# Kernel tuning notes

Hardware: AMD Instinct MI355X
Metric: run time of the kernel (lower is better)

## Reference

```python
import jax, jax.numpy as jnp
import numpy as np

# Sizes (see shape_source): N samples, D=Config.dim, H=D//2, E question types, C classes/type
N, D, H, E, C = 65536, 768, 384, 8, 8


def setup_inputs() -> dict:
    key = jax.random.key(0)
    k_x, k_t, k_w1, k_w2 = jax.random.split(key, 4)
    x = jax.random.normal(k_x, (N, D), dtype=jnp.float32)
    question_types = jax.random.randint(k_t, (N,), 0, E, dtype=jnp.int32)
    # Stacked per-type MLP head parameters (E experts)
    W1 = jax.random.normal(k_w1, (E, D, H), dtype=jnp.float32) * 0.02
    b1 = jnp.zeros((E, H), dtype=jnp.float32)
    W2 = jax.random.normal(k_w2, (E, H, C), dtype=jnp.float32) * 0.02
    b2 = jnp.zeros((E, C), dtype=jnp.float32)
    return {"x": x, "W1": W1, "b1": b1, "W2": W2, "b2": b2,
            "question_types": question_types}


def reference(x, W1, b1, W2, b2, question_types):
    # Per-sample routed 2-layer MLP head: logits_i = MLP_{type_i}(x_i).
    # Dropout is eval-mode identity. Dense-per-expert compute + mask select
    # (standard MoE reference; E is a small fixed loop, not a data-dim loop).
    n_experts = W1.shape[0]
    out = jnp.zeros((x.shape[0], W2.shape[-1]), dtype=x.dtype)
    for e in range(n_experts):
        h = jax.nn.relu(x @ W1[e] + b1[e])        # [N, H]
        logits = h @ W2[e] + b2[e]                # [N, C]
        out = jnp.where((question_types == e)[:, None], logits, out)
    return out
```

## Files before the change

kernel.cpp:

```cpp
#include <hip/hip_runtime.h>

typedef short s16x8 __attribute__((ext_vector_type(8)));
typedef float f32x4 __attribute__((ext_vector_type(4)));

#define N_SAMPLES 65536
#define DIM 768
#define HID 384
#define NEXP 8
#define NCLS 8
#define JT 24
#define KT 24

#define WS_CNT    0
#define WS_BUCKET 1024
#define WS_W1F    (WS_BUCKET + NEXP * N_SAMPLES * 4)

__device__ __forceinline__ unsigned short f2bf(float f) {
  union { float f; unsigned u; } v; v.f = f;
  unsigned r = v.u + 0x7fffu + ((v.u >> 16) & 1u);
  return (unsigned short)(r >> 16);
}

__device__ __forceinline__ unsigned cvt2(float a, float b) {
  union { float f; unsigned u; } ua, ub;
  ua.f = a; ub.f = b;
  return __builtin_amdgcn_perm(ub.u + 0x8000u, ua.u + 0x8000u, 0x07060302u);
}

#define LBAR asm volatile("s_waitcnt lgkmcnt(0)\n\ts_barrier" ::: "memory")

__global__ void k_w1frag(const float* __restrict__ W1,
                         unsigned short* __restrict__ W1F,
                         int* __restrict__ cnt) {
  if (blockIdx.x == 0 && blockIdx.y == 0 && threadIdx.x < NEXP)
    cnt[threadIdx.x] = 0;
  const int e = blockIdx.x;
  const int unit = blockIdx.y * 4 + (threadIdx.x >> 6);
  const int lane = threadIdx.x & 63;
  const int jt = unit / KT, kt = unit % KT;
  const int j = jt * 16 + (lane & 15);
  const int k0 = kt * 32 + (lane >> 4) * 8;
  const float* src = W1 + ((size_t)e * DIM + k0) * HID + j;
  s16x8 v;
#pragma unroll
  for (int i = 0; i < 8; ++i) v[i] = (short)f2bf(src[(size_t)i * HID]);
  *(s16x8*)&W1F[(((size_t)e * JT * KT + unit) * 64 + lane) * 8] = v;
}

__global__ void k_scatter(const int* __restrict__ qt, int* __restrict__ cnt,
                          int* __restrict__ bucket) {
  __shared__ int lcnt[NEXP], lbase[NEXP];
  const int t = threadIdx.x;
  const int i = blockIdx.x * 256 + t;
  if (t < NEXP) lcnt[t] = 0;
  __syncthreads();
  const int e = qt[i];
  const int rank = atomicAdd(&lcnt[e], 1);
  __syncthreads();
  if (t < NEXP) lbase[t] = atomicAdd(&cnt[t], lcnt[t]);
  __syncthreads();
  bucket[(size_t)e * N_SAMPLES + lbase[e] + rank] = i;
}


#define ALOADN(S, KS)                                       \
  { const float4* p_ = (const float4*)(ap + (KS) * 32);     \
    aLo##S = p_[0]; aHi##S = p_[1]; }

#define ASTOREN(BUF, S)                                                     \
  { unsigned q0 = cvt2(aLo##S.x, aLo##S.y), q1 = cvt2(aLo##S.z, aLo##S.w),  \
             q2 = cvt2(aHi##S.x, aHi##S.y), q3 = cvt2(aHi##S.z, aHi##S.w);  \
    uint4 pk_ = {q0, q1, q2, q3};                                           \
    *(uint4*)&(BUF)[ar * 40 + aq * 8] = pk_; }

#define WLOADN(WF, KS)                                                      \
  _Pragma("unroll") for (int ni = 0; ni < 6; ++ni)                          \
      WF[ni] = *(const s16x8*)(wfbase + ((size_t)ni * KT + (KS)) * 512);

#define COMPUTE(AS, WF)                                                     \
  { _Pragma("unroll") for (int mi = 0; mi < 4; ++mi) {                      \
      s16x8 xfr = *(const s16x8*)&(AS)[(mi * 16 + lrow) * 40 + quad * 8];   \
      _Pragma("unroll") for (int ni = 0; ni < 6; ++ni)                      \
          acc[mi][ni] = __builtin_amdgcn_mfma_f32_16x16x32_bf16(            \
              WF[ni], xfr, acc[mi][ni], 0, 0, 0); } }

#define KSTEP(ASC, ASN, SN, SF, KA, WF, KW) \
  ASTOREN(ASN, SN)                          \
  ALOADN(SF, KA)                            \
  COMPUTE(ASC, WF)                          \
  WLOADN(WF, KW)                            \
  LBAR;

__global__ __launch_bounds__(256, 2) void k_moe_gemm(
    const float* __restrict__ x, const unsigned short* __restrict__ W1F,
    const float* __restrict__ b1, const float* __restrict__ W2,
    const float* __restrict__ b2, const int* __restrict__ cnt,
    const int* __restrict__ bucket, float* __restrict__ out) {
  __shared__ __align__(16) short smem[25088];
  __shared__ __align__(16) short W2s[16 * 392];
  __shared__ float b1s[HID];
  __shared__ float b2s[NCLS];
  short* As0 = smem;
  short* As1 = smem + 2560;
  short* Hs  = smem;

  const int e = blockIdx.x;
  const int n_e = cnt[e];
  if (n_e <= 0) return;
  const int t = threadIdx.x;
  const int lane = t & 63;
  const int wave = t >> 6;
  const int lrow = lane & 15;
  const int quad = lane >> 4;
  const int ar = t >> 2;
  const int aq = t & 3;

  for (int j = t; j < HID; j += 256) {
    b1s[j] = b1[e * HID + j];
    const float* wr = W2 + ((size_t)e * HID + j) * NCLS;
#pragma unroll
    for (int c = 0; c < NCLS; ++c) W2s[c * 392 + j] = (short)f2bf(wr[c]);
#pragma unroll
    for (int c = NCLS; c < 16; ++c) W2s[c * 392 + j] = 0;
  }
  if (t < NCLS) b2s[t] = b2[e * NCLS + t];

  const unsigned short* wfbase =
      W1F + ((size_t)(e * JT + wave * 6) * KT) * 512 + lane * 8;

  int aidx = 0;
  {
    const int rt0 = blockIdx.y;
    if (rt0 * 64 < n_e) {
      int slot = rt0 * 64 + ar;
      if (slot >= n_e) slot = n_e - 1;
      aidx = bucket[(size_t)e * N_SAMPLES + slot];
    }
  }

  for (int rt = blockIdx.y; rt * 64 < n_e; rt += gridDim.y) {
    const int row0 = rt * 64;
    const float* ap = x + (size_t)aidx * DIM + aq * 8;

    f32x4 acc[4][6];
#pragma unroll
    for (int mi = 0; mi < 4; ++mi)
#pragma unroll
      for (int ni = 0; ni < 6; ++ni) acc[mi][ni] = (f32x4){0.f, 0.f, 0.f, 0.f};

    float4 aLo0, aHi0, aLo1, aHi1, aLo2, aHi2, aLo3, aHi3;
    s16x8 wfA[6], wfB[6];

    ALOADN(0, 0) ALOADN(1, 1) ALOADN(2, 2) ALOADN(3, 3)
    WLOADN(wfA, 0) WLOADN(wfB, 1)
    ASTOREN(As0, 0)

    int aidx_n = aidx;
    {
      const int nrt = rt + gridDim.y;
      if (nrt * 64 < n_e) {
        int s = nrt * 64 + ar;
        if (s >= n_e) s = n_e - 1;
        aidx_n = bucket[(size_t)e * N_SAMPLES + s];
      }
    }
    LBAR;

    for (int kb = 0; kb < 20; kb += 4) {
      KSTEP(As0, As1, 1, 0, kb + 4, wfA, kb + 2)
      KSTEP(As1, As0, 2, 1, kb + 5, wfB, kb + 3)
      KSTEP(As0, As1, 3, 2, kb + 6, wfA, kb + 4)
      KSTEP(As1, As0, 0, 3, kb + 7, wfB, kb + 5)
    }

    ASTOREN(As1, 1) COMPUTE(As0, wfA) WLOADN(wfA, 22) LBAR;
    ASTOREN(As0, 2) COMPUTE(As1, wfB) WLOADN(wfB, 23) LBAR;
    ASTOREN(As1, 3) COMPUTE(As0, wfA) LBAR;
    COMPUTE(As1, wfB) LBAR;

#pragma unroll
    for (int mi = 0; mi < 4; ++mi)
#pragma unroll
      for (int ni = 0; ni < 6; ++ni) {
        const int j = wave * 96 + ni * 16 + quad * 4;
        const float4 bb = *(const float4*)&b1s[j];
        float v0 = acc[mi][ni][0] + bb.x; v0 = v0 > 0.f ? v0 : 0.f;
        float v1 = acc[mi][ni][1] + bb.y; v1 = v1 > 0.f ? v1 : 0.f;
        float v2 = acc[mi][ni][2] + bb.z; v2 = v2 > 0.f ? v2 : 0.f;
        float v3 = acc[mi][ni][3] + bb.w; v3 = v3 > 0.f ? v3 : 0.f;
        uint2 pk = {cvt2(v0, v1), cvt2(v2, v3)};
        *(uint2*)&Hs[(mi * 16 + lrow) * 392 + j] = pk;
      }
    LBAR;

    {
      f32x4 acc2 = (f32x4){0.f, 0.f, 0.f, 0.f};
#pragma unroll
      for (int kk = 0; kk < 12; ++kk) {
        s16x8 af = *(const s16x8*)&Hs[(wave * 16 + lrow) * 392 + kk * 32 + quad * 8];
        s16x8 bf = *(const s16x8*)&W2s[lrow * 392 + kk * 32 + quad * 8];
        acc2 = __builtin_amdgcn_mfma_f32_16x16x32_bf16(af, bf, acc2, 0, 0, 0);
      }
      if (lrow < NCLS) {
        const float bb = b2s[lrow];
#pragma unroll
        for (int r = 0; r < 4; ++r) {
          const int m = wave * 16 + quad * 4 + r;
          if (row0 + m < n_e) {
            const int oi = bucket[(size_t)e * N_SAMPLES + row0 + m];
            out[(size_t)oi * NCLS + lrow] = acc2[r] + bb;
          }
        }
      }
    }
    LBAR;
    aidx = aidx_n;
  }
}

extern "C" void kernel_launch(void* const* d_in, const int* in_sizes, int n_in,
                              void* d_out, int out_size, void* d_ws, size_t ws_size,
                              hipStream_t stream) {
  const float* x  = (const float*)d_in[0];
  const float* W1 = (const float*)d_in[1];
  const float* b1 = (const float*)d_in[2];
  const float* W2 = (const float*)d_in[3];
  const float* b2 = (const float*)d_in[4];
  const int* qt   = (const int*)d_in[5];
  float* out = (float*)d_out;
  char* ws = (char*)d_ws;

  int* cnt = (int*)(ws + WS_CNT);
  int* bucket = (int*)(ws + WS_BUCKET);
  unsigned short* W1F = (unsigned short*)(ws + WS_W1F);

  k_w1frag<<<dim3(8, 144), dim3(256), 0, stream>>>(W1, W1F, cnt);
  k_scatter<<<dim3(256), dim3(256), 0, stream>>>(qt, cnt, bucket);
  k_moe_gemm<<<dim3(8, 64), dim3(256), 0, stream>>>(x, W1F, b1, W2, b2, cnt, bucket, out);
}
```

Baseline: 346.1 us.

## Stage activations in larger XOR-swizzled phases with cross-tile prefetch

The activation staging changes from 32-wide K slices, each needing its own barrier, to four 192-wide phases. Each phase is loaded as twelve float4 per thread and stored into an XOR-swizzled LDS layout to avoid bank conflicts. This cuts barriers from about 24 to about 5 per row tile, and the first phase of the next tile is prefetched during the last phase of the current one. In exchange it needs more registers for the 12 float4s and a larger LDS footprint per buffer (12288 shorts), which may pressure occupancy at 2 blocks per CU.

```diff
diff --git a/kernel.cpp b/kernel.cpp
--- a/kernel.cpp
+++ b/kernel.cpp
@@ -10,6 +10,8 @@
 #define NCLS 8
 #define JT 24
 #define KT 24
+#define PHK 6
+#define PHF 192
 
 #define WS_CNT    0
 #define WS_BUCKET 1024
@@ -63,33 +65,40 @@
 }
 
 
-#define ALOADN(S, KS)                                       \
-  { const float4* p_ = (const float4*)(ap + (KS) * 32);     \
-    aLo##S = p_[0]; aHi##S = p_[1]; }
-
-#define ASTOREN(BUF, S)                                                     \
-  { unsigned q0 = cvt2(aLo##S.x, aLo##S.y), q1 = cvt2(aLo##S.z, aLo##S.w),  \
-             q2 = cvt2(aHi##S.x, aHi##S.y), q3 = cvt2(aHi##S.z, aHi##S.w);  \
-    uint4 pk_ = {q0, q1, q2, q3};                                           \
-    *(uint4*)&(BUF)[ar * 40 + aq * 8] = pk_; }
+
+#define ALD(S, I) av##S = app[I];
+#define ALOAD12(APTR, PH)                                                   \
+  { const float4* app = (const float4*)((APTR) + (PH) * PHF + aq * 48);     \
+    ALD(0,0) ALD(1,1) ALD(2,2) ALD(3,3) ALD(4,4) ALD(5,5)                   \
+    ALD(6,6) ALD(7,7) ALD(8,8) ALD(9,9) ALD(10,10) ALD(11,11) }
+
+#define CST(BUF, M, E, O)                                                   \
+  { uint4 pk_ = {cvt2(av##E.x, av##E.y), cvt2(av##E.z, av##E.w),            \
+                 cvt2(av##O.x, av##O.y), cvt2(av##O.z, av##O.w)};           \
+    *(uint4*)&(BUF)[aw_base + (((6 * aq + (M)) ^ arsw) << 3)] = pk_; }
+#define CVTSTORE(BUF) \
+  CST(BUF,0,0,1) CST(BUF,1,2,3) CST(BUF,2,4,5) \
+  CST(BUF,3,6,7) CST(BUF,4,8,9) CST(BUF,5,10,11)
 
 #define WLOADN(WF, KS)                                                      \
   _Pragma("unroll") for (int ni = 0; ni < 6; ++ni)                          \
       WF[ni] = *(const s16x8*)(wfbase + ((size_t)ni * KT + (KS)) * 512);
 
-#define COMPUTE(AS, WF)                                                     \
+#define COMPUTE(AS, WF, KSL)                                                \
   { _Pragma("unroll") for (int mi = 0; mi < 4; ++mi) {                      \
-      s16x8 xfr = *(const s16x8*)&(AS)[(mi * 16 + lrow) * 40 + quad * 8];   \
+      s16x8 xfr = *(const s16x8*)&(AS)[(mi * 16 + lrow) * 192 +             \
+                                       (((((KSL) * 4) + quad) ^ lsw) << 3)];\
       _Pragma("unroll") for (int ni = 0; ni < 6; ++ni)                      \
           acc[mi][ni] = __builtin_amdgcn_mfma_f32_16x16x32_bf16(            \
               WF[ni], xfr, acc[mi][ni], 0, 0, 0); } }
 
-#define KSTEP(ASC, ASN, SN, SF, KA, WF, KW) \
-  ASTOREN(ASN, SN)                          \
-  ALOADN(SF, KA)                            \
-  COMPUTE(ASC, WF)                          \
-  WLOADN(WF, KW)                            \
-  LBAR;
+#define KS(AS, KSG, WF)                                                     \
+  COMPUTE(AS, WF, (KSG) % PHK)                                              \
+  if ((KSG) + 2 < 24) { WLOADN(WF, (KSG) + 2) }
+
+#define PHASE(AS, K0)                                                       \
+  KS(AS, (K0)+0, wfA) KS(AS, (K0)+1, wfB) KS(AS, (K0)+2, wfA)               \
+  KS(AS, (K0)+3, wfB) KS(AS, (K0)+4, wfA) KS(AS, (K0)+5, wfB)
 
 __global__ __launch_bounds__(256, 2) void k_moe_gemm(
     const float* __restrict__ x, const unsigned short* __restrict__ W1F,
@@ -101,7 +110,7 @@
   __shared__ float b1s[HID];
   __shared__ float b2s[NCLS];
   short* As0 = smem;
-  short* As1 = smem + 2560;
+  short* As1 = smem + 12288;
   short* Hs  = smem;
 
   const int e = blockIdx.x;
@@ -114,6 +123,9 @@
   const int quad = lane >> 4;
   const int ar = t >> 2;
   const int aq = t & 3;
+  const int arsw = ar & 7;
+  const int lsw = lrow & 7;
+  const int aw_base = ar * 192;
 
   for (int j = t; j < HID; j += 256) {
     b1s[j] = b1[e * HID + j];
@@ -138,22 +150,17 @@
     }
   }
 
+  float4 av0, av1, av2, av3, av4, av5, av6, av7, av8, av9, av10, av11;
+  s16x8 wfA[6], wfB[6];
+
+  ALOAD12(x + (size_t)aidx * DIM, 0)
+
   for (int rt = blockIdx.y; rt * 64 < n_e; rt += gridDim.y) {
     const int row0 = rt * 64;
-    const float* ap = x + (size_t)aidx * DIM + aq * 8;
-
-    f32x4 acc[4][6];
-#pragma unroll
-    for (int mi = 0; mi < 4; ++mi)
-#pragma unroll
-      for (int ni = 0; ni < 6; ++ni) acc[mi][ni] = (f32x4){0.f, 0.f, 0.f, 0.f};
-
-    float4 aLo0, aHi0, aLo1, aHi1, aLo2, aHi2, aLo3, aHi3;
-    s16x8 wfA[6], wfB[6];
-
-    ALOADN(0, 0) ALOADN(1, 1) ALOADN(2, 2) ALOADN(3, 3)
+    const float* ap = x + (size_t)aidx * DIM;
+
     WLOADN(wfA, 0) WLOADN(wfB, 1)
-    ASTOREN(As0, 0)
+    CVTSTORE(As0)
 
     int aidx_n = aidx;
     {
@@ -164,19 +171,33 @@
         aidx_n = bucket[(size_t)e * N_SAMPLES + s];
       }
     }
-    LBAR;
-
-    for (int kb = 0; kb < 20; kb += 4) {
-      KSTEP(As0, As1, 1, 0, kb + 4, wfA, kb + 2)
-      KSTEP(As1, As0, 2, 1, kb + 5, wfB, kb + 3)
-      KSTEP(As0, As1, 3, 2, kb + 6, wfA, kb + 4)
-      KSTEP(As1, As0, 0, 3, kb + 7, wfB, kb + 5)
-    }
-
-    ASTOREN(As1, 1) COMPUTE(As0, wfA) WLOADN(wfA, 22) LBAR;
-    ASTOREN(As0, 2) COMPUTE(As1, wfB) WLOADN(wfB, 23) LBAR;
-    ASTOREN(As1, 3) COMPUTE(As0, wfA) LBAR;
-    COMPUTE(As1, wfB) LBAR;
+
+    f32x4 acc[4][6];
+#pragma unroll
+    for (int mi = 0; mi < 4; ++mi)
+#pragma unroll
+      for (int ni = 0; ni < 6; ++ni) acc[mi][ni] = (f32x4){0.f, 0.f, 0.f, 0.f};
+
+    LBAR;
+
+    ALOAD12(ap, 1)
+    PHASE(As0, 0)
+    CVTSTORE(As1)
+    LBAR;
+
+    ALOAD12(ap, 2)
+    PHASE(As1, 6)
+    CVTSTORE(As0)
+    LBAR;
+
+    ALOAD12(ap, 3)
+    PHASE(As0, 12)
+    CVTSTORE(As1)
+    LBAR;
+
+    if ((rt + gridDim.y) * 64 < n_e) { ALOAD12(x + (size_t)aidx_n * DIM, 0) }
+    PHASE(As1, 18)
+    LBAR;
 
 #pragma unroll
     for (int mi = 0; mi < 4; ++mi)
```

Measured after the change: 493.5 us. 42.6% more time.

## Stage gathered x rows into LDS via async global_load_lds with swizzle

Applied to the files above, without the earlier changes.

Replaces the register-staged fp32 x loads (load to registers, convert to bf16, store to LDS) with direct global-to-LDS async loads of raw fp32 rows. Each load covers 128 K-elements per phase with an XOR swizzle, and two LDS buffers are double-buffered. Conversion to bf16 moves to the compute step, which reads fp32 from LDS. Explicit vmcnt waits and barriers are hand-scheduled. The aim is to free VGPRs and hide gather latency, at the cost of more LDS (64KB of A buffers), double the LDS read bandwidth, and fragile hand-counted waitcnt values.

```diff
diff --git a/kernel.cpp b/kernel.cpp
--- a/kernel.cpp
+++ b/kernel.cpp
@@ -27,7 +27,16 @@
   return __builtin_amdgcn_perm(ub.u + 0x8000u, ua.u + 0x8000u, 0x07060302u);
 }
 
+#define SBAR  asm volatile("s_barrier" ::: "memory")
+#define MFEN  asm volatile("" ::: "memory")
+#define VMW(N) asm volatile("s_waitcnt vmcnt(" #N ")" ::: "memory")
 #define LBAR asm volatile("s_waitcnt lgkmcnt(0)\n\ts_barrier" ::: "memory")
+
+__device__ __forceinline__ void gload16(const void* g, void* l) {
+  __builtin_amdgcn_global_load_lds(
+      (const __attribute__((address_space(1))) void*)g,
+      (__attribute__((address_space(3))) void*)l, 16, 0, 0);
+}
 
 __global__ void k_w1frag(const float* __restrict__ W1,
                          unsigned short* __restrict__ W1F,
@@ -62,47 +71,54 @@
   bucket[(size_t)e * N_SAMPLES + lbase[e] + rank] = i;
 }
 
-
-#define ALOADN(S, KS)                                       \
-  { const float4* p_ = (const float4*)(ap + (KS) * 32);     \
-    aLo##S = p_[0]; aHi##S = p_[1]; }
-
-#define ASTOREN(BUF, S)                                                     \
-  { unsigned q0 = cvt2(aLo##S.x, aLo##S.y), q1 = cvt2(aLo##S.z, aLo##S.w),  \
-             q2 = cvt2(aHi##S.x, aHi##S.y), q3 = cvt2(aHi##S.z, aHi##S.w);  \
-    uint4 pk_ = {q0, q1, q2, q3};                                           \
-    *(uint4*)&(BUF)[ar * 40 + aq * 8] = pk_; }
+#define GLOADPH(BUF, P)                                                     \
+  _Pragma("unroll") for (int i = 0; i < 8; ++i)                             \
+      gload16((const char*)x + off[i] + (P) * 512,                          \
+              (char*)(BUF) + i * 4096 + wave * 1024);
 
 #define WLOADN(WF, KS)                                                      \
   _Pragma("unroll") for (int ni = 0; ni < 6; ++ni)                          \
       WF[ni] = *(const s16x8*)(wfbase + ((size_t)ni * KT + (KS)) * 512);
 
-#define COMPUTE(AS, WF)                                                     \
+#define COMPUTE4(BUF, WF, KL)                                               \
   { _Pragma("unroll") for (int mi = 0; mi < 4; ++mi) {                      \
-      s16x8 xfr = *(const s16x8*)&(AS)[(mi * 16 + lrow) * 40 + quad * 8];   \
+      const char* rb_ = (const char*)(BUF) + (mi * 16 + lrow) * 512 + (KL) * 128; \
+      float4 c0 = *(const float4*)(rb_ + o0);                               \
+      float4 c1 = *(const float4*)(rb_ + o1);                               \
+      union { uint4 u; s16x8 s; } xf;                                       \
+      xf.u = (uint4){cvt2(c0.x, c0.y), cvt2(c0.z, c0.w),                    \
+                     cvt2(c1.x, c1.y), cvt2(c1.z, c1.w)};                   \
       _Pragma("unroll") for (int ni = 0; ni < 6; ++ni)                      \
           acc[mi][ni] = __builtin_amdgcn_mfma_f32_16x16x32_bf16(            \
-              WF[ni], xfr, acc[mi][ni], 0, 0, 0); } }
-
-#define KSTEP(ASC, ASN, SN, SF, KA, WF, KW) \
-  ASTOREN(ASN, SN)                          \
-  ALOADN(SF, KA)                            \
-  COMPUTE(ASC, WF)                          \
-  WLOADN(WF, KW)                            \
-  LBAR;
+              WF[ni], xf.s, acc[mi][ni], 0, 0, 0); } }
+
+#define KST(BUF, WF, KL, KSG)                                               \
+  COMPUTE4(BUF, WF, KL)                                                     \
+  if ((KSG) + 2 < 24) { WLOADN(WF, (KSG) + 2) }
+
+#define PHASE4(BUF, P)                                                      \
+  KST(BUF, wfA, 0, (P) * 4 + 0)                                             \
+  KST(BUF, wfB, 1, (P) * 4 + 1)                                             \
+  KST(BUF, wfA, 2, (P) * 4 + 2)                                             \
+  KST(BUF, wfB, 3, (P) * 4 + 3)
+
+#define PH_SYNC(BUFC, PN2, VN)                                              \
+  SBAR;                                                                     \
+  GLOADPH(BUFC, PN2)                                                        \
+  VMW(VN); SBAR; MFEN;
 
 __global__ __launch_bounds__(256, 2) void k_moe_gemm(
     const float* __restrict__ x, const unsigned short* __restrict__ W1F,
     const float* __restrict__ b1, const float* __restrict__ W2,
     const float* __restrict__ b2, const int* __restrict__ cnt,
     const int* __restrict__ bucket, float* __restrict__ out) {
-  __shared__ __align__(16) short smem[25088];
+  __shared__ __align__(16) short smem[32768];
   __shared__ __align__(16) short W2s[16 * 392];
   __shared__ float b1s[HID];
   __shared__ float b2s[NCLS];
-  short* As0 = smem;
-  short* As1 = smem + 2560;
-  short* Hs  = smem;
+  float* As0f = (float*)smem;
+  float* As1f = (float*)(smem + 16384);
+  short* Hs = smem;
 
   const int e = blockIdx.x;
   const int n_e = cnt[e];
@@ -112,8 +128,11 @@
   const int wave = t >> 6;
   const int lrow = lane & 15;
   const int quad = lane >> 4;
-  const int ar = t >> 2;
-  const int aq = t & 3;
+  const int lsw = lrow & 7;
+  const int o0 = ((quad * 2) ^ lsw) << 4;
+  const int o1 = o0 ^ 16;
+  const int rbase = wave * 2 + (lane >> 5);
+  const int g16o = (((lane & 31) ^ rbase) << 4);
 
   for (int j = t; j < HID; j += 256) {
     b1s[j] = b1[e * HID + j];
@@ -128,55 +147,46 @@
   const unsigned short* wfbase =
       W1F + ((size_t)(e * JT + wave * 6) * KT) * 512 + lane * 8;
 
-  int aidx = 0;
-  {
-    const int rt0 = blockIdx.y;
-    if (rt0 * 64 < n_e) {
-      int slot = rt0 * 64 + ar;
-      if (slot >= n_e) slot = n_e - 1;
-      aidx = bucket[(size_t)e * N_SAMPLES + slot];
+  unsigned off[8];
+#pragma unroll
+  for (int i = 0; i < 8; ++i) {
+    int s = blockIdx.y * 64 + rbase + 8 * i;
+    if (s >= n_e) s = n_e - 1;
+    off[i] = (unsigned)bucket[(size_t)e * N_SAMPLES + s] * 3072u + g16o;
+  }
+
+  for (int rt = blockIdx.y; rt * 64 < n_e; rt += 64) {
+    const int row0 = rt * 64;
+
+    GLOADPH(As0f, 0)
+    MFEN;
+    GLOADPH(As1f, 1)
+    MFEN;
+    s16x8 wfA[6], wfB[6];
+    WLOADN(wfA, 0)
+    WLOADN(wfB, 1)
+    int nraw[8];
+#pragma unroll
+    for (int i = 0; i < 8; ++i) {
+      int s = row0 + 4096 + rbase + 8 * i;
+      if (s >= n_e) s = n_e - 1;
+      nraw[i] = bucket[(size_t)e * N_SAMPLES + s];
     }
-  }
-
-  for (int rt = blockIdx.y; rt * 64 < n_e; rt += gridDim.y) {
-    const int row0 = rt * 64;
-    const float* ap = x + (size_t)aidx * DIM + aq * 8;
-
     f32x4 acc[4][6];
 #pragma unroll
     for (int mi = 0; mi < 4; ++mi)
 #pragma unroll
       for (int ni = 0; ni < 6; ++ni) acc[mi][ni] = (f32x4){0.f, 0.f, 0.f, 0.f};
-
-    float4 aLo0, aHi0, aLo1, aHi1, aLo2, aHi2, aLo3, aHi3;
-    s16x8 wfA[6], wfB[6];
-
-    ALOADN(0, 0) ALOADN(1, 1) ALOADN(2, 2) ALOADN(3, 3)
-    WLOADN(wfA, 0) WLOADN(wfB, 1)
-    ASTOREN(As0, 0)
-
-    int aidx_n = aidx;
-    {
-      const int nrt = rt + gridDim.y;
-      if (nrt * 64 < n_e) {
-        int s = nrt * 64 + ar;
-        if (s >= n_e) s = n_e - 1;
-        aidx_n = bucket[(size_t)e * N_SAMPLES + s];
-      }
-    }
-    LBAR;
-
-    for (int kb = 0; kb < 20; kb += 4) {
-      KSTEP(As0, As1, 1, 0, kb + 4, wfA, kb + 2)
-      KSTEP(As1, As0, 2, 1, kb + 5, wfB, kb + 3)
-      KSTEP(As0, As1, 3, 2, kb + 6, wfA, kb + 4)
-      KSTEP(As1, As0, 0, 3, kb + 7, wfB, kb + 5)
-    }
-
-    ASTOREN(As1, 1) COMPUTE(As0, wfA) WLOADN(wfA, 22) LBAR;
-    ASTOREN(As0, 2) COMPUTE(As1, wfB) WLOADN(wfB, 23) LBAR;
-    ASTOREN(As1, 3) COMPUTE(As0, wfA) LBAR;
-    COMPUTE(As1, wfB) LBAR;
+    VMW(28); SBAR; MFEN;
+
+    PHASE4(As0f, 0) PH_SYNC(As0f, 2, 52)
+    PHASE4(As1f, 1) PH_SYNC(As1f, 3, 32)
+    PHASE4(As0f, 2) PH_SYNC(As0f, 4, 32)
+    PHASE4(As1f, 3) PH_SYNC(As1f, 5, 32)
+    PHASE4(As0f, 4)
+    SBAR; VMW(24); SBAR; MFEN;
+    PHASE4(As1f, 5)
+    SBAR;
 
 #pragma unroll
     for (int mi = 0; mi < 4; ++mi)
@@ -214,7 +224,9 @@
       }
     }
     LBAR;
-    aidx = aidx_n;
+
+#pragma unroll
+    for (int i = 0; i < 8; ++i) off[i] = (unsigned)nraw[i] * 3072u + g16o;
   }
 }
 
```

After: 473.5 us. 36.8% more time.

## Pre-gather routed rows into contiguous bf16 buffer before expert GEMM

Applied to the files above, without the earlier changes.

Adds a separate gather kernel that copies each expert's routed x rows into a contiguous, expert-sorted bf16 buffer. The GEMM kernel then loads half-width bf16 A tiles straight from that buffer, with no fp32-to-bf16 conversion and no per-row bucket index chasing. The cost is an extra kernel launch plus a full write and re-read of a 96MB bf16 copy of x, in exchange for cheaper, more regular loads in the GEMM.

```diff
diff --git a/kernel.cpp b/kernel.cpp
--- a/kernel.cpp
+++ b/kernel.cpp
@@ -14,6 +14,7 @@
 #define WS_CNT    0
 #define WS_BUCKET 1024
 #define WS_W1F    (WS_BUCKET + NEXP * N_SAMPLES * 4)
+#define WS_XG     (WS_W1F + 8 * 576 * 64 * 8 * 2)
 
 __device__ __forceinline__ unsigned short f2bf(float f) {
   union { float f; unsigned u; } v; v.f = f;
@@ -62,16 +63,53 @@
   bucket[(size_t)e * N_SAMPLES + lbase[e] + rank] = i;
 }
 
-
-#define ALOADN(S, KS)                                       \
-  { const float4* p_ = (const float4*)(ap + (KS) * 32);     \
-    aLo##S = p_[0]; aHi##S = p_[1]; }
-
-#define ASTOREN(BUF, S)                                                     \
-  { unsigned q0 = cvt2(aLo##S.x, aLo##S.y), q1 = cvt2(aLo##S.z, aLo##S.w),  \
-             q2 = cvt2(aHi##S.x, aHi##S.y), q3 = cvt2(aHi##S.z, aHi##S.w);  \
-    uint4 pk_ = {q0, q1, q2, q3};                                           \
-    *(uint4*)&(BUF)[ar * 40 + aq * 8] = pk_; }
+__global__ __launch_bounds__(256) void k_gather(
+    const float* __restrict__ x, const int* __restrict__ cnt,
+    const int* __restrict__ bucket, unsigned short* __restrict__ xg) {
+  const int e = blockIdx.x;
+  int base = 0, n_e = 0;
+#pragma unroll
+  for (int i = 0; i < NEXP; ++i) {
+    int c = cnt[i];
+    if (i < e) base += c;
+    if (i == e) n_e = c;
+  }
+  const int wave = threadIdx.x >> 6, lane = threadIdx.x & 63;
+
+  for (int rt = blockIdx.y; rt * 64 < n_e; rt += gridDim.y) {
+    const int s0 = rt * 64 + wave * 16;
+    int sl = s0 + (lane & 15);
+    if (sl > n_e - 1) sl = n_e - 1;
+    const int bkt = bucket[(size_t)e * N_SAMPLES + sl];
+#pragma unroll
+    for (int r = 0; r < 16; r += 2) {
+      const int sA = s0 + r, sB = s0 + r + 1;
+      const int srcA = __shfl(bkt, r), srcB = __shfl(bkt, r + 1);
+      const float4* pa = (const float4*)(x + (size_t)srcA * DIM);
+      const float4* pb = (const float4*)(x + (size_t)srcB * DIM);
+      float4 c0, c1, c2, c3, c4, c5;
+      if (sA < n_e) { c0 = pa[lane]; c1 = pa[64 + lane]; c2 = pa[128 + lane]; }
+      if (sB < n_e) { c3 = pb[lane]; c4 = pb[64 + lane]; c5 = pb[128 + lane]; }
+      if (sA < n_e) {
+        uint2* da = (uint2*)(xg + (size_t)(base + sA) * DIM);
+        da[lane]       = (uint2){cvt2(c0.x, c0.y), cvt2(c0.z, c0.w)};
+        da[64 + lane]  = (uint2){cvt2(c1.x, c1.y), cvt2(c1.z, c1.w)};
+        da[128 + lane] = (uint2){cvt2(c2.x, c2.y), cvt2(c2.z, c2.w)};
+      }
+      if (sB < n_e) {
+        uint2* db = (uint2*)(xg + (size_t)(base + sB) * DIM);
+        db[lane]       = (uint2){cvt2(c3.x, c3.y), cvt2(c3.z, c3.w)};
+        db[64 + lane]  = (uint2){cvt2(c4.x, c4.y), cvt2(c4.z, c4.w)};
+        db[128 + lane] = (uint2){cvt2(c5.x, c5.y), cvt2(c5.z, c5.w)};
+      }
+    }
+  }
+}
+
+
+#define ALOADN(S, KS) a##S = *(const s16x8*)(ap + (KS) * 32);
+
+#define ASTOREN(BUF, S) *(s16x8*)&(BUF)[ar * 40 + aq * 8] = a##S;
 
 #define WLOADN(WF, KS)                                                      \
   _Pragma("unroll") for (int ni = 0; ni < 6; ++ni)                          \
@@ -92,7 +130,7 @@
   LBAR;
 
 __global__ __launch_bounds__(256, 2) void k_moe_gemm(
-    const float* __restrict__ x, const unsigned short* __restrict__ W1F,
+    const unsigned short* __restrict__ xg, const unsigned short* __restrict__ W1F,
     const float* __restrict__ b1, const float* __restrict__ W2,
     const float* __restrict__ b2, const int* __restrict__ cnt,
     const int* __restrict__ bucket, float* __restrict__ out) {
@@ -105,7 +143,13 @@
   short* Hs  = smem;
 
   const int e = blockIdx.x;
-  const int n_e = cnt[e];
+  int base = 0, n_e = 0;
+#pragma unroll
+  for (int i = 0; i < NEXP; ++i) {
+    int c = cnt[i];
+    if (i < e) base += c;
+    if (i == e) n_e = c;
+  }
   if (n_e <= 0) return;
   const int t = threadIdx.x;
   const int lane = t & 63;
@@ -128,19 +172,11 @@
   const unsigned short* wfbase =
       W1F + ((size_t)(e * JT + wave * 6) * KT) * 512 + lane * 8;
 
-  int aidx = 0;
-  {
-    const int rt0 = blockIdx.y;
-    if (rt0 * 64 < n_e) {
-      int slot = rt0 * 64 + ar;
-      if (slot >= n_e) slot = n_e - 1;
-      aidx = bucket[(size_t)e * N_SAMPLES + slot];
-    }
-  }
-
   for (int rt = blockIdx.y; rt * 64 < n_e; rt += gridDim.y) {
     const int row0 = rt * 64;
-    const float* ap = x + (size_t)aidx * DIM + aq * 8;
+    int rowc = row0 + ar;
+    if (rowc > n_e - 1) rowc = n_e - 1;
+    const unsigned short* ap = xg + (size_t)(base + rowc) * DIM + aq * 8;
 
     f32x4 acc[4][6];
 #pragma unroll
@@ -148,22 +184,12 @@
 #pragma unroll
       for (int ni = 0; ni < 6; ++ni) acc[mi][ni] = (f32x4){0.f, 0.f, 0.f, 0.f};
 
-    float4 aLo0, aHi0, aLo1, aHi1, aLo2, aHi2, aLo3, aHi3;
+    s16x8 a0, a1, a2, a3;
     s16x8 wfA[6], wfB[6];
 
     ALOADN(0, 0) ALOADN(1, 1) ALOADN(2, 2) ALOADN(3, 3)
     WLOADN(wfA, 0) WLOADN(wfB, 1)
     ASTOREN(As0, 0)
-
-    int aidx_n = aidx;
-    {
-      const int nrt = rt + gridDim.y;
-      if (nrt * 64 < n_e) {
-        int s = nrt * 64 + ar;
-        if (s >= n_e) s = n_e - 1;
-        aidx_n = bucket[(size_t)e * N_SAMPLES + s];
-      }
-    }
     LBAR;
 
     for (int kb = 0; kb < 20; kb += 4) {
@@ -214,7 +240,6 @@
       }
     }
     LBAR;
-    aidx = aidx_n;
   }
 }
 
@@ -233,8 +258,10 @@
   int* cnt = (int*)(ws + WS_CNT);
   int* bucket = (int*)(ws + WS_BUCKET);
   unsigned short* W1F = (unsigned short*)(ws + WS_W1F);
+  unsigned short* xg  = (unsigned short*)(ws + WS_XG);
 
   k_w1frag<<<dim3(8, 144), dim3(256), 0, stream>>>(W1, W1F, cnt);
   k_scatter<<<dim3(256), dim3(256), 0, stream>>>(qt, cnt, bucket);
-  k_moe_gemm<<<dim3(8, 64), dim3(256), 0, stream>>>(x, W1F, b1, W2, b2, cnt, bucket, out);
-}
+  k_gather<<<dim3(8, 128), dim3(256), 0, stream>>>(x, cnt, bucket, xg);
+  k_moe_gemm<<<dim3(8, 64), dim3(256), 0, stream>>>(xg, W1F, b1, W2, b2, cnt, bucket, out);
+}
```

Result: slower. 385.4 us (+11.4%).
